# Kernel optimization log

Hardware: AMD Instinct MI355X
Metric: run time of the kernel (lower is better)

Reference implementation:

```python
import jax, jax.numpy as jnp
import numpy as np

D_HEAD = 64

def setup_inputs() -> dict:
    key = jax.random.key(0)
    ks = jax.random.split(key, 5)
    B, N, d_feat, d = 8, 2048, 256, 3
    f = jax.random.normal(ks[0], (B, N, d_feat), dtype=jnp.float32)
    x_tilde = jax.random.normal(ks[1], (B, N, d), dtype=jnp.float32)
    log_eps = jax.random.normal(ks[2], (B,), dtype=jnp.float32)
    W_q = jax.random.normal(ks[3], (d_feat + 1, D_HEAD), dtype=jnp.float32) * (1.0 / np.sqrt(d_feat + 1))
    W_k = jax.random.normal(ks[4], (d_feat + 1, D_HEAD), dtype=jnp.float32) * (1.0 / np.sqrt(d_feat + 1))
    return {"f": f, "x_tilde": x_tilde, "log_eps": log_eps, "W_q": W_q, "W_k": W_k}

def reference(f, x_tilde, log_eps, W_q, W_k):
    B, N, _ = f.shape
    # concat per-cloud log_eps scalar to every particle's features
    le = jnp.broadcast_to(log_eps[:, None, None], (B, N, 1)).astype(f.dtype)
    fc = jnp.concatenate([f, le], axis=-1)            # (B, N, d_feat+1)
    q = jnp.einsum('bnf,fh->bnh', fc, W_q)            # (B, N, d_head)
    k = jnp.einsum('bnf,fh->bnh', fc, W_k)            # (B, N, d_head)
    scale = jnp.asarray(np.sqrt(float(D_HEAD)), dtype=f.dtype)
    logits = jnp.einsum('bnh,bmh->bnm', q, k) / scale  # (B, N, N)
    N_f = jnp.asarray(N, dtype=f.dtype)
    col_softmax = jax.nn.softmax(logits, axis=1)       # softmax over QUERY axis
    pi = col_softmax / N_f                             # (B, N, N)
    # y_tilde = N * pi^T @ x_tilde
    y_tilde = N_f * jnp.einsum('bnm,bnd->bmd', pi, x_tilde)  # (B, N, d)
    return y_tilde, pi
```

## Files before the change

kernel.cpp:

```cpp
#include <hip/hip_runtime.h>
#include <hip/hip_bf16.h>

#define BB 8
#define NN 2048
#define DF 256
#define HH 64

using bf16x8 = __attribute__((ext_vector_type(8))) short;
using f32x4  = __attribute__((ext_vector_type(4))) float;
typedef unsigned short u16;

static __device__ __forceinline__ short bf_hi_bits(float v, float* hi_f) {
    __hip_bfloat16 h = __float2bfloat16(v);
    *hi_f = __bfloat162float(h);
    return __builtin_bit_cast(short, h);
}

__global__ __launch_bounds__(64) void wprep_kernel(
    const float* __restrict__ Wq, const float* __restrict__ Wk,
    u16* __restrict__ Wsp)
{
    const int fid  = blockIdx.x;
    const int kc   = fid >> 3, ct = fid & 7;
    const int lane = threadIdx.x;
    const float* W = (ct < 4) ? Wq : Wk;
    const int col  = (ct & 3) * 16 + (lane & 15);
    const int krow = kc * 32 + (lane >> 4) * 8;
    bf16x8 hv, lv;
#pragma unroll
    for (int j = 0; j < 8; ++j) {
        float w = W[(size_t)(krow + j) * HH + col];
        float hf, d;
        hv[j] = bf_hi_bits(w, &hf);
        lv[j] = bf_hi_bits(w - hf, &d);
    }
    u16* dst = Wsp + (size_t)fid * 1024 + lane * 8;
    *(bf16x8*)dst         = hv;
    *(bf16x8*)(dst + 512) = lv;
}

__global__ __launch_bounds__(256) void qk_mfma_kernel(
    const float* __restrict__ f, const float* __restrict__ log_eps,
    const float* __restrict__ Wq, const float* __restrict__ Wk,
    const u16* __restrict__ Wsp,
    __hip_bfloat16* __restrict__ Qs, __hip_bfloat16* __restrict__ Ks)
{
    __shared__ f32x4 red[3 * 64 * 8];

    const int tid  = threadIdx.x;
    const int wave = tid >> 6;
    const int lane = tid & 63;
    const int l15  = lane & 15, quad = lane >> 4;
    const int row0 = blockIdx.x * 16;
    const int b    = row0 >> 11;

    f32x4 acc[8] = {};
    const float* frow = f + (size_t)(row0 + l15) * DF + quad * 8;

#pragma unroll
    for (int kci = 0; kci < 2; ++kci) {
        const int kc = wave * 2 + kci;
        float4 a0 = *(const float4*)(frow + kc * 32);
        float4 a1 = *(const float4*)(frow + kc * 32 + 4);
        bf16x8 ah, al;
#pragma unroll
        for (int e = 0; e < 4; ++e) {
            float hf, d;
            float v0 = (&a0.x)[e], v1 = (&a1.x)[e];
            ah[e]     = bf_hi_bits(v0, &hf);
            al[e]     = bf_hi_bits(v0 - hf, &d);
            ah[e + 4] = bf_hi_bits(v1, &hf);
            al[e + 4] = bf_hi_bits(v1 - hf, &d);
        }
        const u16* wb = Wsp + (size_t)kc * 8192 + lane * 8;
#pragma unroll
        for (int ct = 0; ct < 8; ++ct) {
            bf16x8 bh = *(const bf16x8*)(wb + ct * 1024);
            bf16x8 bl = *(const bf16x8*)(wb + ct * 1024 + 512);
            acc[ct] = __builtin_amdgcn_mfma_f32_16x16x32_bf16(ah, bh, acc[ct], 0, 0, 0);
            acc[ct] = __builtin_amdgcn_mfma_f32_16x16x32_bf16(ah, bl, acc[ct], 0, 0, 0);
            acc[ct] = __builtin_amdgcn_mfma_f32_16x16x32_bf16(al, bh, acc[ct], 0, 0, 0);
        }
    }

    if (wave > 0) {
#pragma unroll
        for (int ct = 0; ct < 8; ++ct)
            red[((wave - 1) * 64 + lane) * 8 + ct] = acc[ct];
    }
    __syncthreads();
    if (wave != 0) return;

#pragma unroll
    for (int ct = 0; ct < 8; ++ct)
#pragma unroll
        for (int w = 0; w < 3; ++w) {
            f32x4 p = red[(w * 64 + lane) * 8 + ct];
            acc[ct][0] += p[0]; acc[ct][1] += p[1];
            acc[ct][2] += p[2]; acc[ct][3] += p[3];
        }

    const float le = log_eps[b];
#pragma unroll
    for (int ct = 0; ct < 8; ++ct) {
        const int h = (ct & 3) * 16 + l15;
        const float wlast = (ct < 4 ? Wq : Wk)[DF * HH + h];
        __hip_bfloat16* out = (ct < 4) ? Qs : Ks;
        const float sc = (ct < 4) ? 0.125f : 1.0f;
#pragma unroll
        for (int r = 0; r < 4; ++r) {
            int bn = row0 + quad * 4 + r;
            float v = (acc[ct][r] + le * wlast) * sc;
            __hip_bfloat16 hi = __float2bfloat16(v);
            __hip_bfloat16 lo = __float2bfloat16(v - __bfloat162float(hi));
            out[(size_t)bn * 128 + h]      = hi;
            out[(size_t)bn * 128 + 64 + h] = lo;
        }
    }
}

__global__ __launch_bounds__(512, 2) void attn_kernel(
    const u16* __restrict__ Qs, const u16* __restrict__ Ks,
    const float* __restrict__ x, float* __restrict__ y, float* __restrict__ pi)
{
    __shared__ float xs[NN * 3];
    __shared__ float cred[64];
    __shared__ float yred[8 * 4 * 16 * 3];

    const int tid   = threadIdx.x;
    const int strip = blockIdx.x;
    const int b     = blockIdx.y;
    const int m0    = strip * 64;
    const int wave  = tid >> 6;
    const int lane  = tid & 63;
    const int l15   = lane & 15;
    const int quad  = lane >> 4;

    if (tid < 64) cred[tid] = 0.f;
    for (int i = tid; i < NN * 3; i += 512) xs[i] = x[(size_t)b * NN * 3 + i];
    __syncthreads();

    bf16x8 bh[4][2], bl[4][2];
    {
        const u16* Kb = Ks + ((size_t)b * NN + m0) * 128;
#pragma unroll
        for (int ct = 0; ct < 4; ++ct) {
            const u16* kr = Kb + (size_t)(ct * 16 + l15) * 128;
#pragma unroll
            for (int ks = 0; ks < 2; ++ks) {
                int k0 = ks * 32 + quad * 8;
                bh[ct][ks] = *(const bf16x8*)(kr + k0);
                bl[ct][ks] = *(const bf16x8*)(kr + 64 + k0);
            }
        }
    }

    const u16* Qb = Qs + (size_t)b * NN * 128;
    float cs[4] = {0.f, 0.f, 0.f, 0.f};
    float yacc[4][3] = {};

    for (int rt = 0; rt < 8; ++rt) {
#pragma unroll
        for (int sr = 0; sr < 2; ++sr) {
            const int row0 = rt * 256 + wave * 32 + sr * 16;
            const u16* qr = Qb + (size_t)(row0 + l15) * 128;
            bf16x8 ah[2], al[2];
#pragma unroll
            for (int ks = 0; ks < 2; ++ks) {
                int k0 = ks * 32 + quad * 8;
                ah[ks] = *(const bf16x8*)(qr + k0);
                al[ks] = *(const bf16x8*)(qr + 64 + k0);
            }
            float xv[4][3];
#pragma unroll
            for (int r = 0; r < 4; ++r) {
                int row = row0 + quad * 4 + r;
                xv[r][0] = xs[row * 3 + 0];
                xv[r][1] = xs[row * 3 + 1];
                xv[r][2] = xs[row * 3 + 2];
            }
#pragma unroll
            for (int ct = 0; ct < 4; ++ct) {
                f32x4 acc = {0.f, 0.f, 0.f, 0.f};
#pragma unroll
                for (int ks = 0; ks < 2; ++ks) {
                    acc = __builtin_amdgcn_mfma_f32_16x16x32_bf16(ah[ks], bh[ct][ks], acc, 0, 0, 0);
                    acc = __builtin_amdgcn_mfma_f32_16x16x32_bf16(ah[ks], bl[ct][ks], acc, 0, 0, 0);
                    acc = __builtin_amdgcn_mfma_f32_16x16x32_bf16(al[ks], bh[ct][ks], acc, 0, 0, 0);
                }
                float s = 0.f;
#pragma unroll
                for (int r = 0; r < 4; ++r) {
                    float v = __expf(acc[r]);
                    s += v;
                    yacc[ct][0] = fmaf(v, xv[r][0], yacc[ct][0]);
                    yacc[ct][1] = fmaf(v, xv[r][1], yacc[ct][1]);
                    yacc[ct][2] = fmaf(v, xv[r][2], yacc[ct][2]);
                }
                cs[ct] += s;
            }
        }
    }

#pragma unroll
    for (int ct = 0; ct < 4; ++ct) {
        cs[ct] += __shfl_xor(cs[ct], 16);
        cs[ct] += __shfl_xor(cs[ct], 32);
#pragma unroll
        for (int d = 0; d < 3; ++d) {
            yacc[ct][d] += __shfl_xor(yacc[ct][d], 16);
            yacc[ct][d] += __shfl_xor(yacc[ct][d], 32);
        }
    }
    if (quad == 0) {
#pragma unroll
        for (int ct = 0; ct < 4; ++ct) {
            atomicAdd(&cred[ct * 16 + l15], cs[ct]);
#pragma unroll
            for (int d = 0; d < 3; ++d)
                yred[((wave * 4 + ct) * 16 + l15) * 3 + d] = yacc[ct][d];
        }
    }
    __syncthreads();

    if (tid < 192) {
        int c = tid / 3, d = tid - c * 3;
        int ct = c >> 4, cl = c & 15;
        float s = 0.f;
#pragma unroll
        for (int w = 0; w < 8; ++w)
            s += yred[((w * 4 + ct) * 16 + cl) * 3 + d];
        y[((size_t)b * NN + m0 + c) * 3 + d] = s / cred[c];
    }

    const float invN = 1.0f / (float)NN;
    float iv[4];
#pragma unroll
    for (int ct = 0; ct < 4; ++ct) iv[ct] = invN / cred[ct * 16 + l15];
    float* pib = pi + (size_t)b * NN * NN + m0;

    for (int rt = 0; rt < 8; ++rt) {
#pragma unroll
        for (int sr = 0; sr < 2; ++sr) {
            const int row0 = rt * 256 + wave * 32 + sr * 16;
            const u16* qr = Qb + (size_t)(row0 + l15) * 128;
            bf16x8 ah[2], al[2];
#pragma unroll
            for (int ks = 0; ks < 2; ++ks) {
                int k0 = ks * 32 + quad * 8;
                ah[ks] = *(const bf16x8*)(qr + k0);
                al[ks] = *(const bf16x8*)(qr + 64 + k0);
            }
#pragma unroll
            for (int ct = 0; ct < 4; ++ct) {
                f32x4 acc = {0.f, 0.f, 0.f, 0.f};
#pragma unroll
                for (int ks = 0; ks < 2; ++ks) {
                    acc = __builtin_amdgcn_mfma_f32_16x16x32_bf16(ah[ks], bh[ct][ks], acc, 0, 0, 0);
                    acc = __builtin_amdgcn_mfma_f32_16x16x32_bf16(ah[ks], bl[ct][ks], acc, 0, 0, 0);
                    acc = __builtin_amdgcn_mfma_f32_16x16x32_bf16(al[ks], bh[ct][ks], acc, 0, 0, 0);
                }
                float* op = pib + (size_t)(row0 + quad * 4) * NN + ct * 16 + l15;
#pragma unroll
                for (int r = 0; r < 4; ++r)
                    op[(size_t)r * NN] = __expf(acc[r]) * iv[ct];
            }
        }
    }
}

extern "C" void kernel_launch(void* const* d_in, const int* in_sizes, int n_in,
                              void* d_out, int out_size, void* d_ws, size_t ws_size,
                              hipStream_t stream) {
    const float* f  = (const float*)d_in[0];
    const float* x  = (const float*)d_in[1];
    const float* le = (const float*)d_in[2];
    const float* Wq = (const float*)d_in[3];
    const float* Wk = (const float*)d_in[4];

    float* y  = (float*)d_out;
    float* pi = (float*)d_out + (size_t)BB * NN * 3;

    __hip_bfloat16* Qs = (__hip_bfloat16*)d_ws;
    __hip_bfloat16* Ks = Qs + (size_t)BB * NN * 128;
    u16* Wsp = (u16*)pi;

    wprep_kernel<<<dim3(64), 64, 0, stream>>>(Wq, Wk, Wsp);
    qk_mfma_kernel<<<dim3(BB * NN / 16), 256, 0, stream>>>(f, le, Wq, Wk, Wsp, Qs, Ks);
    attn_kernel<<<dim3(32, BB), 512, 0, stream>>>((const u16*)Qs, (const u16*)Ks,
                                                  x, y, pi);
}
```

Measured before the change: 195.1 us.

## Restructure QK projection to share weight tiles across waves via double-buffered LDS

```diff
diff --git a/kernel.cpp b/kernel.cpp
--- a/kernel.cpp
+++ b/kernel.cpp
@@ -45,23 +45,39 @@
     const u16* __restrict__ Wsp,
     __hip_bfloat16* __restrict__ Qs, __hip_bfloat16* __restrict__ Ks)
 {
-    __shared__ f32x4 red[3 * 64 * 8];
+    __shared__ __align__(16) u16 wbuf[2][8192];
 
     const int tid  = threadIdx.x;
     const int wave = tid >> 6;
     const int lane = tid & 63;
     const int l15  = lane & 15, quad = lane >> 4;
-    const int row0 = blockIdx.x * 16;
-    const int b    = row0 >> 11;
+    const int row0 = blockIdx.x * 64 + wave * 16;
+    const int b    = (blockIdx.x * 64) >> 11;
 
     f32x4 acc[8] = {};
     const float* frow = f + (size_t)(row0 + l15) * DF + quad * 8;
 
-#pragma unroll
-    for (int kci = 0; kci < 2; ++kci) {
-        const int kc = wave * 2 + kci;
-        float4 a0 = *(const float4*)(frow + kc * 32);
-        float4 a1 = *(const float4*)(frow + kc * 32 + 4);
+    {
+        const uint4* src = (const uint4*)(Wsp + tid * 32);
+        uint4* dst = (uint4*)&wbuf[0][tid * 32];
+#pragma unroll
+        for (int i = 0; i < 4; ++i) dst[i] = src[i];
+    }
+    float4 a0 = *(const float4*)(frow);
+    float4 a1 = *(const float4*)(frow + 4);
+    __syncthreads();
+
+    for (int kc = 0; kc < 8; ++kc) {
+        const int cur = kc & 1;
+        uint4 w0, w1, w2, w3;
+        float4 na0, na1;
+        if (kc < 7) {
+            const uint4* src =
+                (const uint4*)(Wsp + (size_t)(kc + 1) * 8192 + tid * 32);
+            w0 = src[0]; w1 = src[1]; w2 = src[2]; w3 = src[3];
+            na0 = *(const float4*)(frow + (kc + 1) * 32);
+            na1 = *(const float4*)(frow + (kc + 1) * 32 + 4);
+        }
         bf16x8 ah, al;
 #pragma unroll
         for (int e = 0; e < 4; ++e) {
@@ -72,33 +88,21 @@
             ah[e + 4] = bf_hi_bits(v1, &hf);
             al[e + 4] = bf_hi_bits(v1 - hf, &d);
         }
-        const u16* wb = Wsp + (size_t)kc * 8192 + lane * 8;
 #pragma unroll
         for (int ct = 0; ct < 8; ++ct) {
-            bf16x8 bh = *(const bf16x8*)(wb + ct * 1024);
-            bf16x8 bl = *(const bf16x8*)(wb + ct * 1024 + 512);
+            bf16x8 bh = *(const bf16x8*)&wbuf[cur][ct * 1024 + lane * 8];
+            bf16x8 bl = *(const bf16x8*)&wbuf[cur][ct * 1024 + 512 + lane * 8];
             acc[ct] = __builtin_amdgcn_mfma_f32_16x16x32_bf16(ah, bh, acc[ct], 0, 0, 0);
             acc[ct] = __builtin_amdgcn_mfma_f32_16x16x32_bf16(ah, bl, acc[ct], 0, 0, 0);
             acc[ct] = __builtin_amdgcn_mfma_f32_16x16x32_bf16(al, bh, acc[ct], 0, 0, 0);
         }
-    }
-
-    if (wave > 0) {
-#pragma unroll
-        for (int ct = 0; ct < 8; ++ct)
-            red[((wave - 1) * 64 + lane) * 8 + ct] = acc[ct];
-    }
-    __syncthreads();
-    if (wave != 0) return;
-
-#pragma unroll
-    for (int ct = 0; ct < 8; ++ct)
-#pragma unroll
-        for (int w = 0; w < 3; ++w) {
-            f32x4 p = red[(w * 64 + lane) * 8 + ct];
-            acc[ct][0] += p[0]; acc[ct][1] += p[1];
-            acc[ct][2] += p[2]; acc[ct][3] += p[3];
-        }
+        if (kc < 7) {
+            uint4* dst = (uint4*)&wbuf[cur ^ 1][tid * 32];
+            dst[0] = w0; dst[1] = w1; dst[2] = w2; dst[3] = w3;
+            a0 = na0; a1 = na1;
+        }
+        __syncthreads();
+    }
 
     const float le = log_eps[b];
 #pragma unroll
@@ -286,7 +290,7 @@
     u16* Wsp = (u16*)pi;
 
     wprep_kernel<<<dim3(64), 64, 0, stream>>>(Wq, Wk, Wsp);
-    qk_mfma_kernel<<<dim3(BB * NN / 16), 256, 0, stream>>>(f, le, Wq, Wk, Wsp, Qs, Ks);
+    qk_mfma_kernel<<<dim3(BB * NN / 64), 256, 0, stream>>>(f, le, Wq, Wk, Wsp, Qs, Ks);
     attn_kernel<<<dim3(32, BB), 512, 0, stream>>>((const u16*)Qs, (const u16*)Ks,
                                                   x, y, pi);
 }
```

After: 194.3 us. No clear change (-0.4%).

## Fuse weight prep, QK projection and attention into one cooperative kernel

Applied to the files above, without the earlier changes.

```diff
diff --git a/kernel.cpp b/kernel.cpp
--- a/kernel.cpp
+++ b/kernel.cpp
@@ -1,5 +1,8 @@
 #include <hip/hip_runtime.h>
 #include <hip/hip_bf16.h>
+#include <hip/hip_cooperative_groups.h>
+
+namespace cg = cooperative_groups;
 
 #define BB 8
 #define NN 2048
@@ -16,125 +19,106 @@
     return __builtin_bit_cast(short, h);
 }
 
-__global__ __launch_bounds__(64) void wprep_kernel(
+__global__ __launch_bounds__(512, 2) void fused_kernel(
+    const float* __restrict__ f, const float* __restrict__ x,
+    const float* __restrict__ log_eps,
     const float* __restrict__ Wq, const float* __restrict__ Wk,
-    u16* __restrict__ Wsp)
-{
-    const int fid  = blockIdx.x;
-    const int kc   = fid >> 3, ct = fid & 7;
-    const int lane = threadIdx.x;
-    const float* W = (ct < 4) ? Wq : Wk;
-    const int col  = (ct & 3) * 16 + (lane & 15);
-    const int krow = kc * 32 + (lane >> 4) * 8;
-    bf16x8 hv, lv;
-#pragma unroll
-    for (int j = 0; j < 8; ++j) {
-        float w = W[(size_t)(krow + j) * HH + col];
-        float hf, d;
-        hv[j] = bf_hi_bits(w, &hf);
-        lv[j] = bf_hi_bits(w - hf, &d);
-    }
-    u16* dst = Wsp + (size_t)fid * 1024 + lane * 8;
-    *(bf16x8*)dst         = hv;
-    *(bf16x8*)(dst + 512) = lv;
-}
-
-__global__ __launch_bounds__(256) void qk_mfma_kernel(
-    const float* __restrict__ f, const float* __restrict__ log_eps,
-    const float* __restrict__ Wq, const float* __restrict__ Wk,
-    const u16* __restrict__ Wsp,
-    __hip_bfloat16* __restrict__ Qs, __hip_bfloat16* __restrict__ Ks)
-{
-    __shared__ f32x4 red[3 * 64 * 8];
-
-    const int tid  = threadIdx.x;
-    const int wave = tid >> 6;
-    const int lane = tid & 63;
-    const int l15  = lane & 15, quad = lane >> 4;
-    const int row0 = blockIdx.x * 16;
-    const int b    = row0 >> 11;
-
-    f32x4 acc[8] = {};
-    const float* frow = f + (size_t)(row0 + l15) * DF + quad * 8;
-
-#pragma unroll
-    for (int kci = 0; kci < 2; ++kci) {
-        const int kc = wave * 2 + kci;
-        float4 a0 = *(const float4*)(frow + kc * 32);
-        float4 a1 = *(const float4*)(frow + kc * 32 + 4);
-        bf16x8 ah, al;
-#pragma unroll
-        for (int e = 0; e < 4; ++e) {
-            float hf, d;
-            float v0 = (&a0.x)[e], v1 = (&a1.x)[e];
-            ah[e]     = bf_hi_bits(v0, &hf);
-            al[e]     = bf_hi_bits(v0 - hf, &d);
-            ah[e + 4] = bf_hi_bits(v1, &hf);
-            al[e + 4] = bf_hi_bits(v1 - hf, &d);
-        }
-        const u16* wb = Wsp + (size_t)kc * 8192 + lane * 8;
-#pragma unroll
-        for (int ct = 0; ct < 8; ++ct) {
-            bf16x8 bh = *(const bf16x8*)(wb + ct * 1024);
-            bf16x8 bl = *(const bf16x8*)(wb + ct * 1024 + 512);
-            acc[ct] = __builtin_amdgcn_mfma_f32_16x16x32_bf16(ah, bh, acc[ct], 0, 0, 0);
-            acc[ct] = __builtin_amdgcn_mfma_f32_16x16x32_bf16(ah, bl, acc[ct], 0, 0, 0);
-            acc[ct] = __builtin_amdgcn_mfma_f32_16x16x32_bf16(al, bh, acc[ct], 0, 0, 0);
-        }
-    }
-
-    if (wave > 0) {
-#pragma unroll
-        for (int ct = 0; ct < 8; ++ct)
-            red[((wave - 1) * 64 + lane) * 8 + ct] = acc[ct];
-    }
-    __syncthreads();
-    if (wave != 0) return;
-
-#pragma unroll
-    for (int ct = 0; ct < 8; ++ct)
-#pragma unroll
-        for (int w = 0; w < 3; ++w) {
-            f32x4 p = red[(w * 64 + lane) * 8 + ct];
-            acc[ct][0] += p[0]; acc[ct][1] += p[1];
-            acc[ct][2] += p[2]; acc[ct][3] += p[3];
-        }
-
-    const float le = log_eps[b];
-#pragma unroll
-    for (int ct = 0; ct < 8; ++ct) {
-        const int h = (ct & 3) * 16 + l15;
-        const float wlast = (ct < 4 ? Wq : Wk)[DF * HH + h];
-        __hip_bfloat16* out = (ct < 4) ? Qs : Ks;
-        const float sc = (ct < 4) ? 0.125f : 1.0f;
-#pragma unroll
-        for (int r = 0; r < 4; ++r) {
-            int bn = row0 + quad * 4 + r;
-            float v = (acc[ct][r] + le * wlast) * sc;
-            __hip_bfloat16 hi = __float2bfloat16(v);
-            __hip_bfloat16 lo = __float2bfloat16(v - __bfloat162float(hi));
-            out[(size_t)bn * 128 + h]      = hi;
-            out[(size_t)bn * 128 + 64 + h] = lo;
-        }
-    }
-}
-
-__global__ __launch_bounds__(512, 2) void attn_kernel(
-    const u16* __restrict__ Qs, const u16* __restrict__ Ks,
-    const float* __restrict__ x, float* __restrict__ y, float* __restrict__ pi)
+    u16* __restrict__ Qs, u16* __restrict__ Ks,
+    float* __restrict__ y, float* __restrict__ pi)
 {
     __shared__ float xs[NN * 3];
     __shared__ float cred[64];
     __shared__ float yred[8 * 4 * 16 * 3];
 
-    const int tid   = threadIdx.x;
-    const int strip = blockIdx.x;
-    const int b     = blockIdx.y;
+    cg::grid_group grid = cg::this_grid();
+
+    const int tid  = threadIdx.x;
+    const int bid  = blockIdx.x;
+    const int wave = tid >> 6;
+    const int lane = tid & 63;
+    const int l15  = lane & 15;
+    const int quad = lane >> 4;
+
+    u16* Wsp = (u16*)pi;
+
+    if (bid < 8) {
+        const int fid = bid * 8 + wave;
+        const int kc = fid >> 3, ct = fid & 7;
+        const float* W = (ct < 4) ? Wq : Wk;
+        const int col  = (ct & 3) * 16 + l15;
+        const int krow = kc * 32 + quad * 8;
+        bf16x8 hv, lv;
+#pragma unroll
+        for (int j = 0; j < 8; ++j) {
+            float w = W[(size_t)(krow + j) * HH + col];
+            float hf, d;
+            hv[j] = bf_hi_bits(w, &hf);
+            lv[j] = bf_hi_bits(w - hf, &d);
+        }
+        u16* dst = Wsp + (size_t)fid * 1024 + lane * 8;
+        *(bf16x8*)dst         = hv;
+        *(bf16x8*)(dst + 512) = lv;
+    }
+    grid.sync();
+
+    {
+        const int t = bid * 8 + wave;
+        if (t < 1024) {
+            const int row0 = t * 16;
+            const int b    = row0 >> 11;
+            f32x4 acc[8] = {};
+            const float* frow = f + (size_t)(row0 + l15) * DF + quad * 8;
+
+#pragma unroll
+            for (int kc = 0; kc < 8; ++kc) {
+                float4 a0 = *(const float4*)(frow + kc * 32);
+                float4 a1 = *(const float4*)(frow + kc * 32 + 4);
+                bf16x8 ah, al;
+#pragma unroll
+                for (int e = 0; e < 4; ++e) {
+                    float hf, d;
+                    float v0 = (&a0.x)[e], v1 = (&a1.x)[e];
+                    ah[e]     = bf_hi_bits(v0, &hf);
+                    al[e]     = bf_hi_bits(v0 - hf, &d);
+                    ah[e + 4] = bf_hi_bits(v1, &hf);
+                    al[e + 4] = bf_hi_bits(v1 - hf, &d);
+                }
+                const u16* wb = Wsp + (size_t)kc * 8192 + lane * 8;
+#pragma unroll
+                for (int ct = 0; ct < 8; ++ct) {
+                    bf16x8 bh = *(const bf16x8*)(wb + ct * 1024);
+                    bf16x8 bl = *(const bf16x8*)(wb + ct * 1024 + 512);
+                    acc[ct] = __builtin_amdgcn_mfma_f32_16x16x32_bf16(ah, bh, acc[ct], 0, 0, 0);
+                    acc[ct] = __builtin_amdgcn_mfma_f32_16x16x32_bf16(ah, bl, acc[ct], 0, 0, 0);
+                    acc[ct] = __builtin_amdgcn_mfma_f32_16x16x32_bf16(al, bh, acc[ct], 0, 0, 0);
+                }
+            }
+
+            const float le = log_eps[b];
+#pragma unroll
+            for (int ct = 0; ct < 8; ++ct) {
+                const int h = (ct & 3) * 16 + l15;
+                const float wlast = (ct < 4 ? Wq : Wk)[DF * HH + h];
+                u16* out = (ct < 4) ? Qs : Ks;
+                const float sc = (ct < 4) ? 0.125f : 1.0f;
+#pragma unroll
+                for (int r = 0; r < 4; ++r) {
+                    int bn = row0 + quad * 4 + r;
+                    float v = (acc[ct][r] + le * wlast) * sc;
+                    float hf, d;
+                    short hb = bf_hi_bits(v, &hf);
+                    short lb = bf_hi_bits(v - hf, &d);
+                    out[(size_t)bn * 128 + h]      = (u16)hb;
+                    out[(size_t)bn * 128 + 64 + h] = (u16)lb;
+                }
+            }
+        }
+    }
+    grid.sync();
+
+    const int strip = bid >> 3;
+    const int b     = bid & 7;
     const int m0    = strip * 64;
-    const int wave  = tid >> 6;
-    const int lane  = tid & 63;
-    const int l15   = lane & 15;
-    const int quad  = lane >> 4;
 
     if (tid < 64) cred[tid] = 0.f;
     for (int i = tid; i < NN * 3; i += 512) xs[i] = x[(size_t)b * NN * 3 + i];
@@ -281,12 +265,11 @@
     float* y  = (float*)d_out;
     float* pi = (float*)d_out + (size_t)BB * NN * 3;
 
-    __hip_bfloat16* Qs = (__hip_bfloat16*)d_ws;
-    __hip_bfloat16* Ks = Qs + (size_t)BB * NN * 128;
-    u16* Wsp = (u16*)pi;
-
-    wprep_kernel<<<dim3(64), 64, 0, stream>>>(Wq, Wk, Wsp);
-    qk_mfma_kernel<<<dim3(BB * NN / 16), 256, 0, stream>>>(f, le, Wq, Wk, Wsp, Qs, Ks);
-    attn_kernel<<<dim3(32, BB), 512, 0, stream>>>((const u16*)Qs, (const u16*)Ks,
-                                                  x, y, pi);
+    u16* Qs = (u16*)d_ws;
+    u16* Ks = Qs + (size_t)BB * NN * 128;
+
+    void* args[] = {(void*)&f, (void*)&x, (void*)&le, (void*)&Wq, (void*)&Wk,
+                    (void*)&Qs, (void*)&Ks, (void*)&y, (void*)&pi};
+    hipLaunchCooperativeKernel((const void*)fused_kernel, dim3(256), dim3(512),
+                               args, 0, stream);
 }
```

Measured after the change: 261.5 us. 1.34x slower.
